# Performance work log

Measured on AMD Instinct MI355X. Metric: run time of the kernel, lower is better.

## Reference

```python
import jax, jax.numpy as jnp
import numpy as np

VOCAB = 91557
WORD_DIM = 512
HIDDEN = 1024
B, T = 256, 128


def lstm_maxpool(x_emb, W_ih, W_hh, b_ih, b_hh):
    """x_emb: [B, T, D]. PyTorch LSTMCell recurrence (zero init state),
    then elementwise max over time of the hidden states."""
    Bq = x_emb.shape[0]
    H = W_hh.shape[1]

    def step(carry, x_t):
        h, c = carry
        gates = x_t @ W_ih.T + b_ih + h @ W_hh.T + b_hh  # [B, 4H]
        i, f, g, o = jnp.split(gates, 4, axis=-1)  # PyTorch gate order i,f,g,o
        i = jax.nn.sigmoid(i)
        f = jax.nn.sigmoid(f)
        g = jnp.tanh(g)
        o = jax.nn.sigmoid(o)
        c = f * c + i * g
        h = o * jnp.tanh(c)
        return (h, c), h

    h0 = jnp.zeros((Bq, H), x_emb.dtype)
    (_h, _c), hs = jax.lax.scan(step, (h0, h0), jnp.swapaxes(x_emb, 0, 1))  # hs: [T, B, H]
    return jnp.max(hs, axis=0)  # [B, H]


def setup_inputs() -> dict:
    key = jax.random.key(0)
    ks = jax.random.split(key, 9)
    question = jax.random.randint(ks[0], (B, T), 0, VOCAB)
    sentence = jax.random.randint(ks[1], (B, T), 0, VOCAB)
    emb = jax.random.normal(ks[2], (VOCAB, WORD_DIM), dtype=jnp.float32) * 0.02
    W_ih = jax.random.normal(ks[3], (4 * HIDDEN, WORD_DIM), dtype=jnp.float32) * 0.02
    W_hh = jax.random.normal(ks[4], (4 * HIDDEN, HIDDEN), dtype=jnp.float32) * 0.02
    b_ih = jax.random.normal(ks[5], (4 * HIDDEN,), dtype=jnp.float32) * 0.02
    b_hh = jax.random.normal(ks[6], (4 * HIDDEN,), dtype=jnp.float32) * 0.02
    W_last = jax.random.normal(ks[7], (2, 2 * HIDDEN), dtype=jnp.float32) * 0.02
    b_last = jax.random.normal(ks[8], (2,), dtype=jnp.float32) * 0.02
    return {
        "question": question, "sentence": sentence,
        "emb": emb, "W_ih": W_ih, "W_hh": W_hh, "b_ih": b_ih, "b_hh": b_hh,
        "W_last": W_last, "b_last": b_last,
    }


def reference(question, sentence, emb, W_ih, W_hh, b_ih, b_hh, W_last, b_last):
    q_embedded = emb[question]  # [B, T, D]
    s_embedded = emb[sentence]  # [B, T, D]
    hq = lstm_maxpool(q_embedded, W_ih, W_hh, b_ih, b_hh)  # [B, H]
    hs = lstm_maxpool(s_embedded, W_ih, W_hh, b_ih, b_hh)  # [B, H]
    out = jnp.concatenate([hq, hs], axis=1) @ W_last.T + b_last  # [B, 2]
    return jax.nn.sigmoid(out)
```

## Files before the change

kernel.cpp:

```cpp
#include <hip/hip_runtime.h>
#include <hip/hip_bf16.h>
#include <cstdint>


typedef __bf16 bf16x8 __attribute__((ext_vector_type(8)));
typedef float f32x4 __attribute__((ext_vector_type(4)));

__device__ __forceinline__ float sigm(float x) {
    return 1.0f / (1.0f + __expf(-x));
}
__device__ __forceinline__ float tanh_fast(float x) {
    x = fminf(15.0f, fmaxf(-15.0f, x));
    float e = __expf(2.0f * x);
    return (e - 1.0f) / (e + 1.0f);
}
__device__ __forceinline__ ushort f2bu(float f) {
    __hip_bfloat16 h = __float2bfloat16(f);
    return __builtin_bit_cast(unsigned short, h);
}
__device__ __forceinline__ float bu2f(ushort u) {
    return __uint_as_float(((unsigned)u) << 16);
}
__device__ __forceinline__ void gl_lds16(const void* g, void* l) {
    __builtin_amdgcn_global_load_lds(
        (const __attribute__((address_space(1))) unsigned int*)g,
        (__attribute__((address_space(3))) unsigned int*)l, 16, 0, 0);
}

__global__ void prep_weights(const float* __restrict__ Wih,
                             const float* __restrict__ Whh,
                             const float* __restrict__ bih,
                             const float* __restrict__ bhh,
                             __hip_bfloat16* __restrict__ WcT,
                             float* __restrict__ biasc) {
    int p = blockIdx.y;
    int k = blockIdx.x * blockDim.x + threadIdx.x;
    int r = (p & 3) * 1024 + (p >> 2);
    float v = (k < 512) ? Wih[(size_t)r * 512 + k]
                        : Whh[(size_t)r * 1024 + (k - 512)];
    WcT[(size_t)p * 1536 + k] = __float2bfloat16(v);
    if (k == 0) biasc[p] = bih[r] + bhh[r];
}

__global__ void gather_embed(const int* __restrict__ q,
                             const int* __restrict__ s,
                             const float* __restrict__ emb,
                             ushort* __restrict__ X) {
    int rb = blockIdx.x;
    int t = rb >> 9;
    int b = rb & 511;
    int tok = (b < 256) ? q[b * 128 + t] : s[(b - 256) * 128 + t];
    const float2* src = (const float2*)(emb + (size_t)tok * 512);
    ushort2* dst = (ushort2*)(X + (size_t)rb * 512);
    float2 v = src[threadIdx.x];
    ushort2 o;
    o.x = f2bu(v.x);
    o.y = f2bu(v.y);
    dst[threadIdx.x] = o;
}

__global__ void init_state(float* __restrict__ C, float* __restrict__ HMAX,
                           ushort* __restrict__ H0) {
    int i = blockIdx.x * 256 + threadIdx.x;
    C[i] = 0.0f;
    HMAX[i] = -1e30f;
    H0[i] = 0;
}

__global__ __launch_bounds__(256, 2) void xproj_gemm(
    const ushort* __restrict__ X,
    const ushort* __restrict__ WcT,
    ushort* __restrict__ Xb,
    int row0) {
    __shared__ __align__(16) ushort As[128 * 128];
    __shared__ __align__(16) ushort Bs[128 * 128];

    const int tid = threadIdx.x;
    const int n0 = blockIdx.x * 128;
    const int m0 = blockIdx.y * 128;
    const int lane = tid & 63;
    const int w = tid >> 6;
    const int quad = lane >> 4;
    const int l16 = lane & 15;
    const int wm = (w >> 1) * 64;
    const int wn = (w & 1) * 64;

    f32x4 acc[4][4] = {};

    for (int it = 0; it < 4; ++it) {
        const int k0 = it * 128;
        __syncthreads();
#pragma unroll
        for (int i = 0; i < 8; ++i) {
            int u = i * 256 + tid;
            int r = u >> 4;
            int cs = (u & 15) ^ (r & 15);
            gl_lds16(X + (size_t)(row0 + m0 + r) * 512 + k0 + cs * 8,
                     (ushort*)As + (size_t)u * 8);
            gl_lds16(WcT + (size_t)(n0 + r) * 1536 + k0 + cs * 8,
                     (ushort*)Bs + (size_t)u * 8);
        }
        __syncthreads();
#pragma unroll
        for (int kb = 0; kb < 4; ++kb) {
            bf16x8 af[4], bfr[4];
            const int vsel = (kb << 2) | quad;
#pragma unroll
            for (int mi = 0; mi < 4; ++mi)
                af[mi] = *(const bf16x8*)(As +
                    (((wm + mi * 16 + l16) << 4) + (vsel ^ l16)) * 8);
#pragma unroll
            for (int ni = 0; ni < 4; ++ni)
                bfr[ni] = *(const bf16x8*)(Bs +
                    (((wn + ni * 16 + l16) << 4) + (vsel ^ l16)) * 8);
#pragma unroll
            for (int mi = 0; mi < 4; ++mi)
#pragma unroll
                for (int ni = 0; ni < 4; ++ni)
                    acc[mi][ni] = __builtin_amdgcn_mfma_f32_16x16x32_bf16(
                        af[mi], bfr[ni], acc[mi][ni], 0, 0, 0);
        }
    }

#pragma unroll
    for (int mi = 0; mi < 4; ++mi)
#pragma unroll
        for (int ni = 0; ni < 4; ++ni)
#pragma unroll
            for (int rg = 0; rg < 4; ++rg)
                Xb[(size_t)(m0 + wm + mi * 16 + quad * 4 + rg) * 4096 +
                   (n0 + wn + ni * 16 + l16)] = f2bu(acc[mi][ni][rg]);
}

__global__ __launch_bounds__(256, 2) void lstm_step(
    const ushort* __restrict__ Xb,
    const ushort* __restrict__ WcT,
    const float* __restrict__ biasc,
    const ushort* __restrict__ Hin,
    ushort* __restrict__ Hout,
    float* __restrict__ C,
    float* __restrict__ HMAX,
    int t) {
    __shared__ __align__(16) ushort As[64 * 128];
    __shared__ __align__(16) ushort Bs[128 * 128];
    __shared__ float Gs[64][132];
    __shared__ float biasS[128];

    const int tid = threadIdx.x;
    const int n0 = blockIdx.x * 128;
    const int m0 = blockIdx.y * 64;

    if (tid < 128) biasS[tid] = biasc[n0 + tid];

    const int lane = tid & 63;
    const int w = tid >> 6;
    const int quad = lane >> 4;
    const int l16 = lane & 15;
    const int wm = (w >> 1) * 32;
    const int wn = (w & 1) * 64;

    f32x4 acc[2][4] = {};

    for (int it = 0; it < 8; ++it) {
        const int k0 = it * 128;
        __syncthreads();
#pragma unroll
        for (int i = 0; i < 4; ++i) {
            int u = i * 256 + tid;
            int r = u >> 4;
            int cs = (u & 15) ^ (r & 15);
            gl_lds16(Hin + (size_t)(m0 + r) * 1024 + k0 + cs * 8,
                     (ushort*)As + (size_t)u * 8);
        }
#pragma unroll
        for (int i = 0; i < 8; ++i) {
            int u = i * 256 + tid;
            int r = u >> 4;
            int cs = (u & 15) ^ (r & 15);
            gl_lds16(WcT + (size_t)(n0 + r) * 1536 + 512 + k0 + cs * 8,
                     (ushort*)Bs + (size_t)u * 8);
        }
        __syncthreads();
#pragma unroll
        for (int kb = 0; kb < 4; ++kb) {
            bf16x8 af[2], bfr[4];
            const int vsel = (kb << 2) | quad;
#pragma unroll
            for (int mi = 0; mi < 2; ++mi)
                af[mi] = *(const bf16x8*)(As +
                    (((wm + mi * 16 + l16) << 4) + (vsel ^ l16)) * 8);
#pragma unroll
            for (int ni = 0; ni < 4; ++ni)
                bfr[ni] = *(const bf16x8*)(Bs +
                    (((wn + ni * 16 + l16) << 4) + (vsel ^ l16)) * 8);
#pragma unroll
            for (int mi = 0; mi < 2; ++mi)
#pragma unroll
                for (int ni = 0; ni < 4; ++ni)
                    acc[mi][ni] = __builtin_amdgcn_mfma_f32_16x16x32_bf16(
                        af[mi], bfr[ni], acc[mi][ni], 0, 0, 0);
        }
    }

#pragma unroll
    for (int mi = 0; mi < 2; ++mi)
#pragma unroll
        for (int ni = 0; ni < 4; ++ni)
#pragma unroll
            for (int rg = 0; rg < 4; ++rg)
                Gs[wm + mi * 16 + quad * 4 + rg][wn + ni * 16 + l16] =
                    acc[mi][ni][rg];
    __syncthreads();

    const int m = tid >> 2;
    const int c4 = tid & 3;
    const int col0 = c4 * 32;
    const size_t hrow = (size_t)(m0 + m) * 1024;
    const int j0 = (n0 >> 2) + c4 * 8;
    const ushort* xp =
        Xb + (size_t)((t & 7) * 512 + m0 + m) * 4096 + n0 + col0;

    f32x4 cold0 = *(const f32x4*)&C[hrow + j0];
    f32x4 cold1 = *(const f32x4*)&C[hrow + j0 + 4];
    f32x4 hm0 = *(const f32x4*)&HMAX[hrow + j0];
    f32x4 hm1 = *(const f32x4*)&HMAX[hrow + j0 + 4];
    f32x4 cn0, cn1;
    ushort4 hb0, hb1;
#pragma unroll
    for (int u = 0; u < 8; ++u) {
        int cb = col0 + 4 * u;
        float gi = Gs[m][cb + 0] + bu2f(xp[4 * u + 0]) + biasS[cb + 0];
        float gf = Gs[m][cb + 1] + bu2f(xp[4 * u + 1]) + biasS[cb + 1];
        float gg = Gs[m][cb + 2] + bu2f(xp[4 * u + 2]) + biasS[cb + 2];
        float go = Gs[m][cb + 3] + bu2f(xp[4 * u + 3]) + biasS[cb + 3];
        float iv = sigm(gi);
        float fv = sigm(gf);
        float gv = tanh_fast(gg);
        float ov = sigm(go);
        float cold = (u < 4) ? cold0[u & 3] : cold1[u & 3];
        float cn = fv * cold + iv * gv;
        float h = ov * tanh_fast(cn);
        ushort hbits = f2bu(h);
        if (u < 4) {
            cn0[u & 3] = cn;
            hm0[u & 3] = fmaxf(hm0[u & 3], h);
            ((ushort*)&hb0)[u & 3] = hbits;
        } else {
            cn1[u & 3] = cn;
            hm1[u & 3] = fmaxf(hm1[u & 3], h);
            ((ushort*)&hb1)[u & 3] = hbits;
        }
    }
    *(f32x4*)&C[hrow + j0] = cn0;
    *(f32x4*)&C[hrow + j0 + 4] = cn1;
    *(f32x4*)&HMAX[hrow + j0] = hm0;
    *(f32x4*)&HMAX[hrow + j0 + 4] = hm1;
    *(ushort4*)&Hout[hrow + j0] = hb0;
    *(ushort4*)&Hout[hrow + j0 + 4] = hb1;
}

__global__ void final_out(const float* __restrict__ HMAX,
                          const float* __restrict__ Wl,
                          const float* __restrict__ bl,
                          float* __restrict__ out) {
    int b = blockIdx.x;
    int tid = threadIdx.x;
    float s0 = 0.0f, s1 = 0.0f;
    for (int j = tid; j < 1024; j += 256) {
        float hq = HMAX[(size_t)b * 1024 + j];
        float hs = HMAX[(size_t)(256 + b) * 1024 + j];
        s0 += hq * Wl[j] + hs * Wl[1024 + j];
        s1 += hq * Wl[2048 + j] + hs * Wl[3072 + j];
    }
    __shared__ float r0[256], r1[256];
    r0[tid] = s0;
    r1[tid] = s1;
    __syncthreads();
    for (int off = 128; off > 0; off >>= 1) {
        if (tid < off) {
            r0[tid] += r0[tid + off];
            r1[tid] += r1[tid + off];
        }
        __syncthreads();
    }
    if (tid == 0) {
        out[b * 2 + 0] = sigm(r0[0] + bl[0]);
        out[b * 2 + 1] = sigm(r1[0] + bl[1]);
    }
}

extern "C" void kernel_launch(void* const* d_in, const int* in_sizes, int n_in,
                              void* d_out, int out_size, void* d_ws,
                              size_t ws_size, hipStream_t stream) {
    const int* q = (const int*)d_in[0];
    const int* s = (const int*)d_in[1];
    const float* emb = (const float*)d_in[2];
    const float* Wih = (const float*)d_in[3];
    const float* Whh = (const float*)d_in[4];
    const float* bih = (const float*)d_in[5];
    const float* bhh = (const float*)d_in[6];
    const float* Wl = (const float*)d_in[7];
    const float* bl = (const float*)d_in[8];
    float* out = (float*)d_out;

    char* ws = (char*)d_ws;
    __hip_bfloat16* WcT = (__hip_bfloat16*)(ws + 0);
    float* biasc = (float*)(ws + 12582912);
    ushort* X = (ushort*)(ws + 12599296);
    ushort* Xb = (ushort*)(ws + 79708160);
    ushort* H0 = (ushort*)(ws + 113262592);
    ushort* H1 = (ushort*)(ws + 114311168);
    float* C = (float*)(ws + 115359744);
    float* HMAX = (float*)(ws + 117456896);

    prep_weights<<<dim3(6, 4096), 256, 0, stream>>>(Wih, Whh, bih, bhh, WcT,
                                                    biasc);
    gather_embed<<<65536, 256, 0, stream>>>(q, s, emb, X);
    init_state<<<2048, 256, 0, stream>>>(C, HMAX, H0);

    ushort* hin = H0;
    ushort* hout = H1;
    for (int c = 0; c < 16; ++c) {
        xproj_gemm<<<dim3(32, 32), 256, 0, stream>>>(X, (const ushort*)WcT, Xb,
                                                     c * 4096);
        for (int tt = 0; tt < 8; ++tt) {
            int t = c * 8 + tt;
            lstm_step<<<dim3(32, 8), 256, 0, stream>>>(
                Xb, (const ushort*)WcT, biasc, hin, hout, C, HMAX, t);
            ushort* tmp = hin;
            hin = hout;
            hout = tmp;
        }
    }
    final_out<<<256, 256, 0, stream>>>(HMAX, Wl, bl, out);
}
```

Before: 2.509 ms.

## Fuse 16 LSTM steps into persistent cooperative kernel with grid barriers

Replaces per-timestep lstm_step launches with a cooperative persistent kernel that runs 16 timesteps per launch. Each block keeps its slice of W_hh resident in LDS, holds the cell state and running max in registers, and synchronises with the other blocks through per-row-group atomic counters. The weights are reordered so each block's gate columns line up with its hidden units, which removes the LDS gate staging. Embedding gather and input projection are now done per 16-step chunk, which shrinks the workspace. The aim is to remove launch overhead and repeated weight loads per step, at the cost of spin-wait barriers with a bounded guard that could silently break ordering on timeout.

```diff
diff --git a/kernel.cpp b/kernel.cpp
--- a/kernel.cpp
+++ b/kernel.cpp
@@ -35,7 +35,9 @@
                              float* __restrict__ biasc) {
     int p = blockIdx.y;
     int k = blockIdx.x * blockDim.x + threadIdx.x;
-    int r = (p & 3) * 1024 + (p >> 2);
+    int g = (p >> 4) & 3;
+    int j = ((p >> 6) << 4) | (p & 15);
+    int r = g * 1024 + j;
     float v = (k < 512) ? Wih[(size_t)r * 512 + k]
                         : Whh[(size_t)r * 1024 + (k - 512)];
     WcT[(size_t)p * 1536 + k] = __float2bfloat16(v);
@@ -45,13 +47,13 @@
 __global__ void gather_embed(const int* __restrict__ q,
                              const int* __restrict__ s,
                              const float* __restrict__ emb,
-                             ushort* __restrict__ X) {
+                             ushort* __restrict__ Xc, int t0) {
     int rb = blockIdx.x;
-    int t = rb >> 9;
+    int t = t0 + (rb >> 9);
     int b = rb & 511;
     int tok = (b < 256) ? q[b * 128 + t] : s[(b - 256) * 128 + t];
     const float2* src = (const float2*)(emb + (size_t)tok * 512);
-    ushort2* dst = (ushort2*)(X + (size_t)rb * 512);
+    ushort2* dst = (ushort2*)(Xc + (size_t)rb * 512);
     float2 v = src[threadIdx.x];
     ushort2 o;
     o.x = f2bu(v.x);
@@ -60,18 +62,19 @@
 }
 
 __global__ void init_state(float* __restrict__ C, float* __restrict__ HMAX,
-                           ushort* __restrict__ H0) {
+                           ushort* __restrict__ H0,
+                           unsigned int* __restrict__ bar) {
     int i = blockIdx.x * 256 + threadIdx.x;
     C[i] = 0.0f;
     HMAX[i] = -1e30f;
     H0[i] = 0;
+    if (i < 16) bar[i] = 0;
 }
 
 __global__ __launch_bounds__(256, 2) void xproj_gemm(
     const ushort* __restrict__ X,
     const ushort* __restrict__ WcT,
-    ushort* __restrict__ Xb,
-    int row0) {
+    ushort* __restrict__ Xb) {
     __shared__ __align__(16) ushort As[128 * 128];
     __shared__ __align__(16) ushort Bs[128 * 128];
 
@@ -95,7 +98,7 @@
             int u = i * 256 + tid;
             int r = u >> 4;
             int cs = (u & 15) ^ (r & 15);
-            gl_lds16(X + (size_t)(row0 + m0 + r) * 512 + k0 + cs * 8,
+            gl_lds16(X + (size_t)(m0 + r) * 512 + k0 + cs * 8,
                      (ushort*)As + (size_t)u * 8);
             gl_lds16(WcT + (size_t)(n0 + r) * 1536 + k0 + cs * 8,
                      (ushort*)Bs + (size_t)u * 8);
@@ -125,138 +128,168 @@
 #pragma unroll
     for (int mi = 0; mi < 4; ++mi)
 #pragma unroll
-        for (int ni = 0; ni < 4; ++ni)
-#pragma unroll
-            for (int rg = 0; rg < 4; ++rg)
-                Xb[(size_t)(m0 + wm + mi * 16 + quad * 4 + rg) * 4096 +
-                   (n0 + wn + ni * 16 + l16)] = f2bu(acc[mi][ni][rg]);
-}
-
-__global__ __launch_bounds__(256, 2) void lstm_step(
+        for (int rg = 0; rg < 4; ++rg) {
+            ushort4 v;
+            v.x = f2bu(acc[mi][0][rg]);
+            v.y = f2bu(acc[mi][1][rg]);
+            v.z = f2bu(acc[mi][2][rg]);
+            v.w = f2bu(acc[mi][3][rg]);
+            *(ushort4*)&Xb[(size_t)(m0 + wm + mi * 16 + quad * 4 + rg) * 4096 +
+                           (n0 + wn + l16 * 4)] = v;
+        }
+}
+
+__global__ __launch_bounds__(256, 1) void lstm_chunk(
     const ushort* __restrict__ Xb,
     const ushort* __restrict__ WcT,
     const float* __restrict__ biasc,
-    const ushort* __restrict__ Hin,
-    ushort* __restrict__ Hout,
+    ushort* __restrict__ H0,
+    ushort* __restrict__ H1,
     float* __restrict__ C,
     float* __restrict__ HMAX,
-    int t) {
-    __shared__ __align__(16) ushort As[64 * 128];
-    __shared__ __align__(16) ushort Bs[128 * 128];
-    __shared__ float Gs[64][132];
-    __shared__ float biasS[128];
+    unsigned int* __restrict__ bar,
+    int chunk) {
+    __shared__ __align__(16) ushort Bs[64 * 1024];
 
     const int tid = threadIdx.x;
-    const int n0 = blockIdx.x * 128;
-    const int m0 = blockIdx.y * 64;
-
-    if (tid < 128) biasS[tid] = biasc[n0 + tid];
-
+    const int bid = blockIdx.x;
+    const int xcd = bid & 7;
+    const int slot = bid >> 3;
+    const int rg = xcd >> 1;
+    const int ct = ((xcd & 1) << 5) | slot;
+    const int m0 = rg * 128;
+    const int n0 = ct * 64;
     const int lane = tid & 63;
     const int w = tid >> 6;
     const int quad = lane >> 4;
     const int l16 = lane & 15;
-    const int wm = (w >> 1) * 32;
-    const int wn = (w & 1) * 64;
-
-    f32x4 acc[2][4] = {};
-
-    for (int it = 0; it < 8; ++it) {
-        const int k0 = it * 128;
-        __syncthreads();
-#pragma unroll
-        for (int i = 0; i < 4; ++i) {
-            int u = i * 256 + tid;
-            int r = u >> 4;
-            int cs = (u & 15) ^ (r & 15);
-            gl_lds16(Hin + (size_t)(m0 + r) * 1024 + k0 + cs * 8,
-                     (ushort*)As + (size_t)u * 8);
-        }
-#pragma unroll
-        for (int i = 0; i < 8; ++i) {
-            int u = i * 256 + tid;
-            int r = u >> 4;
-            int cs = (u & 15) ^ (r & 15);
-            gl_lds16(WcT + (size_t)(n0 + r) * 1536 + 512 + k0 + cs * 8,
-                     (ushort*)Bs + (size_t)u * 8);
-        }
-        __syncthreads();
-#pragma unroll
-        for (int kb = 0; kb < 4; ++kb) {
-            bf16x8 af[2], bfr[4];
-            const int vsel = (kb << 2) | quad;
+
+#pragma unroll
+    for (int i = 0; i < 32; ++i) {
+        int ulin = i * 256 + tid;
+        int r = ulin >> 7;
+        int v = (ulin & 0x70) | ((ulin & 15) ^ (r & 15));
+        gl_lds16(WcT + (size_t)(n0 + r) * 1536 + 512 + v * 8,
+                 (ushort*)Bs + (size_t)ulin * 8);
+    }
+
+    float bgate[4];
+#pragma unroll
+    for (int g = 0; g < 4; ++g) bgate[g] = biasc[n0 + g * 16 + l16];
+
+    const int jg = ct * 16 + l16;
+    float creg[2][4], hmx[2][4];
+#pragma unroll
+    for (int mi = 0; mi < 2; ++mi)
+#pragma unroll
+        for (int r4 = 0; r4 < 4; ++r4) {
+            int row = m0 + w * 32 + mi * 16 + quad * 4 + r4;
+            creg[mi][r4] = C[(size_t)row * 1024 + jg];
+            hmx[mi][r4] = HMAX[(size_t)row * 1024 + jg];
+        }
+
+    ushort4 xq[2][4];
+#pragma unroll
+    for (int mi = 0; mi < 2; ++mi)
+#pragma unroll
+        for (int r4 = 0; r4 < 4; ++r4) {
+            int row = m0 + w * 32 + mi * 16 + quad * 4 + r4;
+            xq[mi][r4] =
+                *(const ushort4*)(Xb + (size_t)row * 4096 + n0 + l16 * 4);
+        }
+
+    __syncthreads();
+
+    const ushort* hin = H0;
+    ushort* hout = H1;
+
+#pragma unroll 1
+    for (int tt = 0; tt < 16; ++tt) {
+        f32x4 acc[2][4] = {};
+        const ushort* arow =
+            hin + (size_t)(m0 + w * 32 + l16) * 1024 + quad * 8;
+#pragma unroll 8
+        for (int kt = 0; kt < 32; ++kt) {
+            bf16x8 af0 = *(const bf16x8*)(arow + kt * 32);
+            bf16x8 af1 = *(const bf16x8*)(arow + 16 * 1024 + kt * 32);
+            bf16x8 bq[4];
+            const int v = kt * 4 + quad;
+#pragma unroll
+            for (int ni = 0; ni < 4; ++ni) {
+                int r = ni * 16 + l16;
+                int off = r * 128 + (v & 0x70) + ((v & 15) ^ l16);
+                bq[ni] = *(const bf16x8*)((ushort*)Bs + (size_t)off * 8);
+            }
+#pragma unroll
+            for (int ni = 0; ni < 4; ++ni) {
+                acc[0][ni] = __builtin_amdgcn_mfma_f32_16x16x32_bf16(
+                    af0, bq[ni], acc[0][ni], 0, 0, 0);
+                acc[1][ni] = __builtin_amdgcn_mfma_f32_16x16x32_bf16(
+                    af1, bq[ni], acc[1][ni], 0, 0, 0);
+            }
+        }
+
+#pragma unroll
+        for (int mi = 0; mi < 2; ++mi)
+#pragma unroll
+            for (int r4 = 0; r4 < 4; ++r4) {
+                float gi = acc[mi][0][r4] + bu2f(xq[mi][r4].x) + bgate[0];
+                float gf = acc[mi][1][r4] + bu2f(xq[mi][r4].y) + bgate[1];
+                float gg = acc[mi][2][r4] + bu2f(xq[mi][r4].z) + bgate[2];
+                float go = acc[mi][3][r4] + bu2f(xq[mi][r4].w) + bgate[3];
+                float iv = sigm(gi);
+                float fv = sigm(gf);
+                float gv = tanh_fast(gg);
+                float ov = sigm(go);
+                float cn = fv * creg[mi][r4] + iv * gv;
+                float h = ov * tanh_fast(cn);
+                creg[mi][r4] = cn;
+                hmx[mi][r4] = fmaxf(hmx[mi][r4], h);
+                int row = m0 + w * 32 + mi * 16 + quad * 4 + r4;
+                hout[(size_t)row * 1024 + jg] = f2bu(h);
+            }
+
+        if (tt < 15) {
+            __syncthreads();
+            if (tid == 0)
+                __hip_atomic_fetch_add(&bar[rg], 1u, __ATOMIC_RELEASE,
+                                       __HIP_MEMORY_SCOPE_AGENT);
 #pragma unroll
             for (int mi = 0; mi < 2; ++mi)
-                af[mi] = *(const bf16x8*)(As +
-                    (((wm + mi * 16 + l16) << 4) + (vsel ^ l16)) * 8);
-#pragma unroll
-            for (int ni = 0; ni < 4; ++ni)
-                bfr[ni] = *(const bf16x8*)(Bs +
-                    (((wn + ni * 16 + l16) << 4) + (vsel ^ l16)) * 8);
-#pragma unroll
-            for (int mi = 0; mi < 2; ++mi)
-#pragma unroll
-                for (int ni = 0; ni < 4; ++ni)
-                    acc[mi][ni] = __builtin_amdgcn_mfma_f32_16x16x32_bf16(
-                        af[mi], bfr[ni], acc[mi][ni], 0, 0, 0);
+#pragma unroll
+                for (int r4 = 0; r4 < 4; ++r4) {
+                    int row =
+                        (tt + 1) * 512 + m0 + w * 32 + mi * 16 + quad * 4 + r4;
+                    xq[mi][r4] = *(const ushort4*)(Xb + (size_t)row * 4096 +
+                                                   n0 + l16 * 4);
+                }
+            if (tid == 0) {
+                unsigned target = 64u * (unsigned)(chunk * 15 + tt + 1);
+                int guard = 0;
+                while (__hip_atomic_load(&bar[rg], __ATOMIC_RELAXED,
+                                         __HIP_MEMORY_SCOPE_AGENT) < target &&
+                       guard < (1 << 18)) {
+                    ++guard;
+                    __builtin_amdgcn_s_sleep(2);
+                }
+            }
+            __syncthreads();
+            (void)__hip_atomic_load(&bar[rg], __ATOMIC_ACQUIRE,
+                                    __HIP_MEMORY_SCOPE_AGENT);
+            const ushort* tmp = hin;
+            hin = hout;
+            hout = (ushort*)tmp;
         }
     }
 
 #pragma unroll
     for (int mi = 0; mi < 2; ++mi)
 #pragma unroll
-        for (int ni = 0; ni < 4; ++ni)
-#pragma unroll
-            for (int rg = 0; rg < 4; ++rg)
-                Gs[wm + mi * 16 + quad * 4 + rg][wn + ni * 16 + l16] =
-                    acc[mi][ni][rg];
-    __syncthreads();
-
-    const int m = tid >> 2;
-    const int c4 = tid & 3;
-    const int col0 = c4 * 32;
-    const size_t hrow = (size_t)(m0 + m) * 1024;
-    const int j0 = (n0 >> 2) + c4 * 8;
-    const ushort* xp =
-        Xb + (size_t)((t & 7) * 512 + m0 + m) * 4096 + n0 + col0;
-
-    f32x4 cold0 = *(const f32x4*)&C[hrow + j0];
-    f32x4 cold1 = *(const f32x4*)&C[hrow + j0 + 4];
-    f32x4 hm0 = *(const f32x4*)&HMAX[hrow + j0];
-    f32x4 hm1 = *(const f32x4*)&HMAX[hrow + j0 + 4];
-    f32x4 cn0, cn1;
-    ushort4 hb0, hb1;
-#pragma unroll
-    for (int u = 0; u < 8; ++u) {
-        int cb = col0 + 4 * u;
-        float gi = Gs[m][cb + 0] + bu2f(xp[4 * u + 0]) + biasS[cb + 0];
-        float gf = Gs[m][cb + 1] + bu2f(xp[4 * u + 1]) + biasS[cb + 1];
-        float gg = Gs[m][cb + 2] + bu2f(xp[4 * u + 2]) + biasS[cb + 2];
-        float go = Gs[m][cb + 3] + bu2f(xp[4 * u + 3]) + biasS[cb + 3];
-        float iv = sigm(gi);
-        float fv = sigm(gf);
-        float gv = tanh_fast(gg);
-        float ov = sigm(go);
-        float cold = (u < 4) ? cold0[u & 3] : cold1[u & 3];
-        float cn = fv * cold + iv * gv;
-        float h = ov * tanh_fast(cn);
-        ushort hbits = f2bu(h);
-        if (u < 4) {
-            cn0[u & 3] = cn;
-            hm0[u & 3] = fmaxf(hm0[u & 3], h);
-            ((ushort*)&hb0)[u & 3] = hbits;
-        } else {
-            cn1[u & 3] = cn;
-            hm1[u & 3] = fmaxf(hm1[u & 3], h);
-            ((ushort*)&hb1)[u & 3] = hbits;
-        }
-    }
-    *(f32x4*)&C[hrow + j0] = cn0;
-    *(f32x4*)&C[hrow + j0 + 4] = cn1;
-    *(f32x4*)&HMAX[hrow + j0] = hm0;
-    *(f32x4*)&HMAX[hrow + j0 + 4] = hm1;
-    *(ushort4*)&Hout[hrow + j0] = hb0;
-    *(ushort4*)&Hout[hrow + j0 + 4] = hb1;
+        for (int r4 = 0; r4 < 4; ++r4) {
+            int row = m0 + w * 32 + mi * 16 + quad * 4 + r4;
+            C[(size_t)row * 1024 + jg] = creg[mi][r4];
+            HMAX[(size_t)row * 1024 + jg] = hmx[mi][r4];
+        }
 }
 
 __global__ void final_out(const float* __restrict__ HMAX,
@@ -306,31 +339,35 @@
     char* ws = (char*)d_ws;
     __hip_bfloat16* WcT = (__hip_bfloat16*)(ws + 0);
     float* biasc = (float*)(ws + 12582912);
-    ushort* X = (ushort*)(ws + 12599296);
-    ushort* Xb = (ushort*)(ws + 79708160);
-    ushort* H0 = (ushort*)(ws + 113262592);
-    ushort* H1 = (ushort*)(ws + 114311168);
-    float* C = (float*)(ws + 115359744);
-    float* HMAX = (float*)(ws + 117456896);
+    ushort* Xc = (ushort*)(ws + 12599296);
+    ushort* Xb = (ushort*)(ws + 20987904);
+    ushort* H0 = (ushort*)(ws + 88096768);
+    ushort* H1 = (ushort*)(ws + 89145344);
+    float* C = (float*)(ws + 90193920);
+    float* HMAX = (float*)(ws + 92291072);
+    unsigned int* bar = (unsigned int*)(ws + 94388224);
 
     prep_weights<<<dim3(6, 4096), 256, 0, stream>>>(Wih, Whh, bih, bhh, WcT,
                                                     biasc);
-    gather_embed<<<65536, 256, 0, stream>>>(q, s, emb, X);
-    init_state<<<2048, 256, 0, stream>>>(C, HMAX, H0);
-
-    ushort* hin = H0;
-    ushort* hout = H1;
-    for (int c = 0; c < 16; ++c) {
-        xproj_gemm<<<dim3(32, 32), 256, 0, stream>>>(X, (const ushort*)WcT, Xb,
-                                                     c * 4096);
-        for (int tt = 0; tt < 8; ++tt) {
-            int t = c * 8 + tt;
-            lstm_step<<<dim3(32, 8), 256, 0, stream>>>(
-                Xb, (const ushort*)WcT, biasc, hin, hout, C, HMAX, t);
-            ushort* tmp = hin;
-            hin = hout;
-            hout = tmp;
-        }
+    init_state<<<2048, 256, 0, stream>>>(C, HMAX, H0, bar);
+
+    for (int c = 0; c < 8; ++c) {
+        gather_embed<<<8192, 256, 0, stream>>>(q, s, emb, Xc, c * 16);
+        xproj_gemm<<<dim3(32, 64), 256, 0, stream>>>(Xc, (const ushort*)WcT,
+                                                     Xb);
+        const ushort* XbA = Xb;
+        const ushort* WcTA = (const ushort*)WcT;
+        const float* biascA = biasc;
+        ushort* H0A = H0;
+        ushort* H1A = H1;
+        float* CA = C;
+        float* HMA = HMAX;
+        unsigned int* barA = bar;
+        int ck = c;
+        void* args[] = {&XbA, &WcTA, &biascA, &H0A, &H1A,
+                        &CA,  &HMA,  &barA,   &ck};
+        hipLaunchCooperativeKernel(reinterpret_cast<const void*>(&lstm_chunk),
+                                   dim3(256), dim3(256), args, 0, stream);
     }
     final_out<<<256, 256, 0, stream>>>(HMAX, Wl, bl, out);
 }
```

Result: slower. 3.980 ms (+58.7%).
